# Performance work log

Hardware: AMD Instinct MI355X
Metric: run time of the kernel (lower is better)

Reference implementation:

```python
import jax, jax.numpy as jnp
import numpy as np
from jax import lax

B, T, V, D, H = 32, 128, 32000, 512, 512


def setup_inputs() -> dict:
    key = jax.random.key(0)
    ks = jax.random.split(key, 8)
    s = 0.05  # keep gate pre-activations in a sane range
    return {
        "dst": jax.random.randint(ks[0], (B, T), 0, V),
        "E": jax.random.normal(ks[1], (V, D), jnp.float32) * s,
        "W_ih": jax.random.normal(ks[2], (4 * H, D + H), jnp.float32) * s,
        "W_hh": jax.random.normal(ks[3], (4 * H, H), jnp.float32) * s,
        "b_ih": jnp.zeros((4 * H,), jnp.float32),
        "b_hh": jnp.zeros((4 * H,), jnp.float32),
        "h0": jax.random.normal(ks[4], (B, H), jnp.float32) * s,
        "c0": jax.random.normal(ks[5], (B, H), jnp.float32) * s,
        "out0": jax.random.normal(ks[6], (B, H), jnp.float32) * s,
    }


def reference(dst, E, W_ih, W_hh, b_ih, b_hh, h0, c0, out0):
    # Embed targets: [B, T, D] -> time-major [T, B, D]
    emb_tbd = jnp.swapaxes(E[dst], 0, 1)

    def step(carry, e_t):
        h, c, out_prev = carry
        # input feeding: concat embedding with previous output -> [B, D+H]
        x = jnp.concatenate([e_t, out_prev], axis=1)
        gates = x @ W_ih.T + b_ih + h @ W_hh.T + b_hh  # [B, 4H]
        i, f, g, o = jnp.split(gates, 4, axis=1)
        i = jax.nn.sigmoid(i)
        f = jax.nn.sigmoid(f)
        g = jnp.tanh(g)
        o = jax.nn.sigmoid(o)
        c_new = f * c + i * g
        h_new = o * jnp.tanh(c_new)
        # attn is identity; dropout disabled (p=0 / eval)
        return (h_new, c_new, h_new), h_new

    _, outs_tbh = lax.scan(step, (h0, c0, out0), emb_tbd)  # [T, B, H]
    out_bth = jnp.swapaxes(outs_tbh, 0, 1)  # [B, T, H]
    # weight-tied projection to vocab + log softmax
    logits = jnp.einsum("bth,vh->btv", out_bth, E)  # [B, T, V]
    return jax.nn.log_softmax(logits, axis=-1)
```

## Files before the change

### kernel.cpp

```cpp
#include <hip/hip_runtime.h>
#include <hip/hip_bf16.h>
#include <math.h>

#define B_ 32
#define T_ 128
#define V_ 32000
#define D_ 512
#define H_ 512

typedef __attribute__((ext_vector_type(8))) short bf16x8;
typedef __attribute__((ext_vector_type(8))) unsigned short u16x8;
typedef __attribute__((ext_vector_type(4))) float f32x4;
typedef __attribute__((ext_vector_type(2))) unsigned long long u64x2;

#define AS1 __attribute__((address_space(1)))
#define AS3 __attribute__((address_space(3)))

__device__ __forceinline__ unsigned short f2bf(float x) {
  unsigned int b = __float_as_uint(x);
  return (unsigned short)((b + 0x7FFFu + ((b >> 16) & 1u)) >> 16);
}
__device__ __forceinline__ float bf2f(unsigned short u) {
  return __uint_as_float(((unsigned int)u) << 16);
}
__device__ __forceinline__ float sigm(float x) { return 1.0f / (1.0f + __expf(-x)); }
__device__ __forceinline__ float tanh_fast(float x) { return 1.0f - 2.0f / (__expf(2.0f * x) + 1.0f); }

__device__ __forceinline__ unsigned long long ald64(const unsigned long long* p) {
  return __hip_atomic_load(p, __ATOMIC_RELAXED, __HIP_MEMORY_SCOPE_AGENT);
}
__device__ __forceinline__ unsigned ald32(const unsigned* p) {
  return __hip_atomic_load(p, __ATOMIC_RELAXED, __HIP_MEMORY_SCOPE_AGENT);
}

__global__ __launch_bounds__(64) void embed_bf_kernel(const int* __restrict__ dst,
                                                      const float* __restrict__ E,
                                                      unsigned short* __restrict__ embbf) {
  int rt = blockIdx.x;
  int t = rt >> 5, b = rt & 31;
  int v = dst[b * T_ + t];
  const float4* src = (const float4*)(E + (size_t)v * D_);
  ushort4* d = (ushort4*)(embbf + (size_t)rt * D_);
  #pragma unroll
  for (int r = 0; r < 2; ++r) {
    float4 x = src[threadIdx.x + r * 64];
    ushort4 o; o.x = f2bf(x.x); o.y = f2bf(x.y); o.z = f2bf(x.z); o.w = f2bf(x.w);
    d[threadIdx.x + r * 64] = o;
  }
}

__global__ void cvt_kernel(const float* __restrict__ in, unsigned short* __restrict__ out, int n4) {
  int stride = gridDim.x * blockDim.x;
  for (int i = blockIdx.x * blockDim.x + threadIdx.x; i < n4; i += stride) {
    float4 v = ((const float4*)in)[i];
    ushort4 o; o.x = f2bf(v.x); o.y = f2bf(v.y); o.z = f2bf(v.z); o.w = f2bf(v.w);
    ((ushort4*)out)[i] = o;
  }
}

__global__ void cvt_w1_kernel(const float* __restrict__ Wih, unsigned short* __restrict__ W1bf, int n4) {
  int stride = gridDim.x * blockDim.x;
  for (int i = blockIdx.x * blockDim.x + threadIdx.x; i < n4; i += stride) {
    int flat = i * 4;
    int r = flat >> 9, c = flat & 511;
    float4 v = *(const float4*)(Wih + (size_t)r * 1024 + c);
    ushort4 o; o.x = f2bf(v.x); o.y = f2bf(v.y); o.z = f2bf(v.z); o.w = f2bf(v.w);
    ((ushort4*)W1bf)[i] = o;
  }
}

__global__ void wr_prep_swz_kernel(const float* __restrict__ Wih, const float* __restrict__ Whh,
                                   unsigned short* __restrict__ Wrs, int n4) {
  int stride = gridDim.x * blockDim.x;
  for (int i = blockIdx.x * blockDim.x + threadIdx.x; i < n4; i += stride) {
    int flat = i * 4;
    int grow = flat >> 9, k = flat & 511;
    float4 a = *(const float4*)(Wih + (size_t)grow * 1024 + 512 + k);
    float4 b = ((const float4*)Whh)[i];
    ushort4 o;
    o.x = f2bf(a.x + b.x); o.y = f2bf(a.y + b.y); o.z = f2bf(a.z + b.z); o.w = f2bf(a.w + b.w);
    int gate = grow >> 9, kgl = grow & 511;
    int orow = (kgl >> 5) * 128 + (kgl & 31) * 4 + gate;
    int chunk = (k >> 3) ^ (orow & 7);
    *(ushort4*)(Wrs + (size_t)orow * 512 + chunk * 8 + (k & 7)) = o;
  }
}

__global__ __launch_bounds__(256) void gemm_pre_kernel(
    const unsigned short* __restrict__ A,
    const unsigned short* __restrict__ Bm,
    const float* __restrict__ bih, const float* __restrict__ bhh,
    unsigned short* __restrict__ preA3)
{
  __shared__ unsigned short ldsA[2][128 * 32];
  __shared__ unsigned short ldsB[2][128 * 32];
  const int tid = threadIdx.x;
  const int lane = tid & 63;
  const int wid = tid >> 6;
  const int wm = wid >> 1, wn = wid & 1;
  const int m0 = blockIdx.y * 128;
  const int n0 = blockIdx.x * 128;
  const int srow = lane >> 2;
  const int scol = (lane & 3) * 8;

  f32x4 acc[4][4] = {};
  const int NK = 512 / 32;

  auto stage = [&](int kk, int buf) {
    const int k0 = kk * 32;
    #pragma unroll
    for (int c = 0; c < 2; ++c) {
      const int r = wid * 32 + c * 16;
      const unsigned short* sa = A  + (size_t)(m0 + r + srow) * 512 + k0 + scol;
      const unsigned short* sb = Bm + (size_t)(n0 + r + srow) * 512 + k0 + scol;
      __builtin_amdgcn_global_load_lds((const AS1 void*)sa, (AS3 void*)&ldsA[buf][r * 32], 16, 0, 0);
      __builtin_amdgcn_global_load_lds((const AS1 void*)sb, (AS3 void*)&ldsB[buf][r * 32], 16, 0, 0);
    }
  };

  stage(0, 0);
  __syncthreads();

  const int rl = lane & 15;
  const int kb = lane >> 4;

  for (int kk = 0; kk < NK; ++kk) {
    const int buf = kk & 1;
    if (kk + 1 < NK) stage(kk + 1, buf ^ 1);
    const bf16x8* Af = (const bf16x8*)&ldsA[buf][0];
    const bf16x8* Bf = (const bf16x8*)&ldsB[buf][0];
    bf16x8 av[4], bv[4];
    #pragma unroll
    for (int mi = 0; mi < 4; ++mi) av[mi] = Af[(wm * 64 + mi * 16 + rl) * 4 + kb];
    #pragma unroll
    for (int ni = 0; ni < 4; ++ni) bv[ni] = Bf[(wn * 64 + ni * 16 + rl) * 4 + kb];
    #pragma unroll
    for (int mi = 0; mi < 4; ++mi)
      #pragma unroll
      for (int ni = 0; ni < 4; ++ni)
        acc[mi][ni] = __builtin_amdgcn_mfma_f32_16x16x32_bf16(av[mi], bv[ni], acc[mi][ni], 0, 0, 0);
    __syncthreads();
  }

  const int rb = (lane >> 4) * 4;
  #pragma unroll
  for (int mi = 0; mi < 4; ++mi)
    #pragma unroll
    for (int ni = 0; ni < 4; ++ni) {
      int mbase = m0 + wm * 64 + mi * 16 + rb;
      int col   = n0 + wn * 64 + ni * 16 + rl;
      int gate = col >> 9, kg = col & 511;
      int tt = mbase >> 5, bb0 = mbase & 31;
      float bb = bih[col] + bhh[col];
      #pragma unroll
      for (int j = 0; j < 4; ++j)
        preA3[(((size_t)tt * 512 + kg) * 32 + bb0 + j) * 4 + gate] = f2bf(acc[mi][ni][j] + bb);
    }
}

__global__ __launch_bounds__(256) void delta0_kernel(const float* __restrict__ Wih,
                                                     const float* __restrict__ out0,
                                                     const float* __restrict__ h0,
                                                     unsigned short* __restrict__ preA3) {
  const int r = blockIdx.x;
  const int tid = threadIdx.x;
  const int b = tid >> 3, seg = tid & 7;
  __shared__ float red[32][9];
  const float4* o4 = (const float4*)(out0 + (size_t)b * 512 + seg * 64);
  const float4* h4 = (const float4*)(h0 + (size_t)b * 512 + seg * 64);
  const float4* w4 = (const float4*)(Wih + (size_t)r * 1024 + 512 + seg * 64);
  float s = 0.f;
  #pragma unroll
  for (int j = 0; j < 16; ++j) {
    float4 o = o4[j], h = h4[j], w = w4[j];
    s += (o.x - h.x) * w.x + (o.y - h.y) * w.y + (o.z - h.z) * w.z + (o.w - h.w) * w.w;
  }
  red[b][seg] = s;
  __syncthreads();
  if (tid < 32) {
    float t = 0.f;
    #pragma unroll
    for (int j = 0; j < 8; ++j) t += red[tid][j];
    int gate = r >> 9, kgl = r & 511;
    unsigned short* p = preA3 + ((size_t)kgl * 32 + tid) * 4 + gate;
    *p = f2bf(bf2f(*p) + t);
  }
}

__global__ __launch_bounds__(1024) void lstm_persist_rs_kernel(
    const unsigned short* __restrict__ Wrs,
    const unsigned short* __restrict__ preA3,
    const float* __restrict__ c0,
    unsigned short* __restrict__ hb0,
    unsigned short* __restrict__ hb1,
    unsigned short* __restrict__ Abf,
    unsigned int* __restrict__ flags)
{
  __shared__ unsigned short wlds[128 * 512];
  __shared__ __align__(16) char hexch[2][16 * 1024];
  const int tid = threadIdx.x, bid = blockIdx.x;
  const int lane = tid & 63, wid = tid >> 6;

  #pragma unroll
  for (int it = 0; it < 8; ++it) {
    int r = it * 16 + wid;
    const unsigned short* src = Wrs + ((size_t)bid * 128 + r) * 512 + lane * 8;
    __builtin_amdgcn_global_load_lds((const AS1 void*)src, (AS3 void*)&wlds[r * 512], 16, 0, 0);
  }

  const int myhalf = wid >> 3;
  const int rt = wid & 7;
  const int q = lane >> 4, rl = lane & 15;
  const int kg = bid * 32 + rt * 4 + q;
  const int b = myhalf * 16 + rl;
  float c_reg = c0[(size_t)b * 512 + kg];

  const int row = rt * 16 + rl;
  const char* wbase = (const char*)wlds + row * 1024;
  const int rx = (row & 7) << 4;
  const int hx = (rl & 7) << 4;

  const int sw = wid & 7;
  const int sr = sw * 2 + (lane >> 5);
  const int sc = lane & 31;
  const int sblk = sc >> 1;
  const int srx = (sr & 7) << 4;
  const int sofs = sc * 32;

  if (myhalf == 0) {
    const unsigned long long* src =
        (const unsigned long long*)(hb0 + (size_t)sr * 512) + sc * 4;
    unsigned long long d0 = ald64(src + 0), d1 = ald64(src + 1);
    unsigned long long d2 = ald64(src + 2), d3 = ald64(src + 3);
    char* dst = hexch[0] + sr * 1024;
    u64x2 w0; w0[0] = d0; w0[1] = d1;
    u64x2 w1; w1[0] = d2; w1[1] = d3;
    *(u64x2*)(dst + (sofs ^ srx)) = w0;
    *(u64x2*)(dst + ((sofs + 16) ^ srx)) = w1;
  }
  __syncthreads();

  for (int p = 0; p < 2 * T_; ++p) {
    const int t = p >> 1, ph = p & 1, buf = p & 1;

    if (myhalf == ph) {
      unsigned long long pre =
          *(const unsigned long long*)(preA3 + (((size_t)t * 512 + kg) * 32 + b) * 4);
      const char* hbase = hexch[buf] + rl * 1024;
      f32x4 acc = {}, acc2 = {};
      #pragma unroll
      for (int kk = 0; kk < 16; kk += 2) {
        int k0 = kk * 32 + q * 8;
        int k1 = k0 + 32;
        bf16x8 av0 = *(const bf16x8*)(wbase + ((k0 * 2) ^ rx));
        bf16x8 bv0 = *(const bf16x8*)(hbase + ((k0 * 2) ^ hx));
        bf16x8 av1 = *(const bf16x8*)(wbase + ((k1 * 2) ^ rx));
        bf16x8 bv1 = *(const bf16x8*)(hbase + ((k1 * 2) ^ hx));
        acc  = __builtin_amdgcn_mfma_f32_16x16x32_bf16(av0, bv0, acc, 0, 0, 0);
        acc2 = __builtin_amdgcn_mfma_f32_16x16x32_bf16(av1, bv1, acc2, 0, 0, 0);
      }
      float g0 = acc[0] + acc2[0] + bf2f((unsigned short)(pre));
      float g1 = acc[1] + acc2[1] + bf2f((unsigned short)(pre >> 16));
      float g2 = acc[2] + acc2[2] + bf2f((unsigned short)(pre >> 32));
      float g3 = acc[3] + acc2[3] + bf2f((unsigned short)(pre >> 48));
      float iv = sigm(g0), fv = sigm(g1), gv = tanh_fast(g2), ov = sigm(g3);
      float cn = fv * c_reg + iv * gv;
      c_reg = cn;
      float hn = ov * tanh_fast(cn);
      int hv = (int)f2bf(hn);
      int nb = __shfl(hv, lane + 16);
      if ((q & 1) == 0) {
        unsigned pair = (unsigned)hv | ((unsigned)nb << 16);
        if (t != T_ - 1) {
          unsigned short* hout = ((t + 1) & 1) ? hb1 : hb0;
          __hip_atomic_store((unsigned int*)(hout + (size_t)b * 512 + kg), pair,
                             __ATOMIC_RELAXED, __HIP_MEMORY_SCOPE_AGENT);
        }
        *(unsigned*)(Abf + ((size_t)b * T_ + t) * 512 + kg) = pair;
      }
    } else if (p + 1 < 2 * T_) {
      const int t2 = (p + 1) >> 1;
      if (t2 > 0) {
        const unsigned* fl = &flags[(myhalf * 16 + sblk) * 16];
        unsigned spins = 0;
        while (ald32(fl) < (unsigned)t2) {
          if (++spins > 1000000u) break;
        }
      }
      const unsigned short* hsrc = (t2 & 1) ? hb1 : hb0;
      const unsigned long long* src =
          (const unsigned long long*)(hsrc + (size_t)(myhalf * 16 + sr) * 512) + sc * 4;
      unsigned long long d0 = ald64(src + 0), d1 = ald64(src + 1);
      unsigned long long d2 = ald64(src + 2), d3 = ald64(src + 3);
      char* dst = hexch[buf ^ 1] + sr * 1024;
      u64x2 w0; w0[0] = d0; w0[1] = d1;
      u64x2 w1; w1[0] = d2; w1[1] = d3;
      *(u64x2*)(dst + (sofs ^ srx)) = w0;
      *(u64x2*)(dst + ((sofs + 16) ^ srx)) = w1;
    }

    __syncthreads();

    if (tid == ph * 512)
      __hip_atomic_store(&flags[(ph * 16 + bid) * 16], (unsigned)(t + 1),
                         __ATOMIC_RELAXED, __HIP_MEMORY_SCOPE_AGENT);
  }
}

__global__ __launch_bounds__(256) void gemm_kernel(
    const unsigned short* __restrict__ A,
    const unsigned short* __restrict__ Bm,
    float* __restrict__ C,
    unsigned short* __restrict__ Cbf,
    int use_bf,
    float* __restrict__ pmax, float* __restrict__ psum)
{
  __shared__ unsigned short ldsA[2][128 * 32];
  __shared__ unsigned short ldsB[2][128 * 32];
  __shared__ float smax[2][128];
  __shared__ float ssum[2][128];
  const int tid = threadIdx.x;
  const int lane = tid & 63;
  const int wid = tid >> 6;
  const int wm = wid >> 1, wn = wid & 1;
  const int m0 = blockIdx.x * 128;
  const int n0 = blockIdx.y * 128;
  const int srow = lane >> 2;

  f32x4 acc[4][4] = {};
  const int NK = 512 / 32;

  auto stage = [&](int kk, int buf) {
    const int k0 = kk * 32;
    const int sw = (srow >> 1) & 3;
    const int gc = ((lane & 3) ^ sw) * 8;
    #pragma unroll
    for (int c = 0; c < 2; ++c) {
      const int r = wid * 32 + c * 16;
      const unsigned short* sa = A  + (size_t)(m0 + r + srow) * 512 + k0 + gc;
      const unsigned short* sb = Bm + (size_t)(n0 + r + srow) * 512 + k0 + gc;
      __builtin_amdgcn_global_load_lds((const AS1 void*)sa, (AS3 void*)&ldsA[buf][r * 32], 16, 0, 0);
      __builtin_amdgcn_global_load_lds((const AS1 void*)sb, (AS3 void*)&ldsB[buf][r * 32], 16, 0, 0);
    }
  };

  stage(0, 0);
  __syncthreads();

  const int rl = lane & 15;
  const int kb = lane >> 4;
  const int rsw = kb ^ ((rl >> 1) & 3);

  for (int kk = 0; kk < NK; ++kk) {
    const int buf = kk & 1;
    if (kk + 1 < NK) stage(kk + 1, buf ^ 1);
    const bf16x8* Af = (const bf16x8*)&ldsA[buf][0];
    const bf16x8* Bf = (const bf16x8*)&ldsB[buf][0];
    bf16x8 av[4], bv[4];
    #pragma unroll
    for (int mi = 0; mi < 4; ++mi) av[mi] = Af[(wm * 64 + mi * 16 + rl) * 4 + rsw];
    #pragma unroll
    for (int ni = 0; ni < 4; ++ni) bv[ni] = Bf[(wn * 64 + ni * 16 + rl) * 4 + rsw];
    #pragma unroll
    for (int mi = 0; mi < 4; ++mi)
      #pragma unroll
      for (int ni = 0; ni < 4; ++ni)
        acc[mi][ni] = __builtin_amdgcn_mfma_f32_16x16x32_bf16(av[mi], bv[ni], acc[mi][ni], 0, 0, 0);
    __syncthreads();
  }

  const int rb = kb * 4;
  if (use_bf) {
    #pragma unroll
    for (int mi = 0; mi < 4; ++mi)
      #pragma unroll
      for (int ni = 0; ni < 4; ++ni) {
        size_t rrow = (size_t)(m0 + wm * 64 + mi * 16 + rb);
        size_t col = (size_t)(n0 + wn * 64 + ni * 16 + rl);
        #pragma unroll
        for (int j = 0; j < 4; ++j)
          __builtin_nontemporal_store(f2bf(acc[mi][ni][j]), &Cbf[(rrow + j) * (size_t)V_ + col]);
      }
  } else {
    #pragma unroll
    for (int mi = 0; mi < 4; ++mi)
      #pragma unroll
      for (int ni = 0; ni < 4; ++ni) {
        size_t rrow = (size_t)(m0 + wm * 64 + mi * 16 + rb);
        size_t col = (size_t)(n0 + wn * 64 + ni * 16 + rl);
        #pragma unroll
        for (int j = 0; j < 4; ++j)
          __builtin_nontemporal_store(acc[mi][ni][j], &C[(rrow + j) * (size_t)V_ + col]);
      }
  }

  float tm[4][4];
  #pragma unroll
  for (int mi = 0; mi < 4; ++mi)
    #pragma unroll
    for (int j = 0; j < 4; ++j) {
      float m = fmaxf(fmaxf(acc[mi][0][j], acc[mi][1][j]), fmaxf(acc[mi][2][j], acc[mi][3][j]));
      m = fmaxf(m, __shfl_xor(m, 1)); m = fmaxf(m, __shfl_xor(m, 2));
      m = fmaxf(m, __shfl_xor(m, 4)); m = fmaxf(m, __shfl_xor(m, 8));
      tm[mi][j] = m;
    }
  if (rl == 0) {
    #pragma unroll
    for (int mi = 0; mi < 4; ++mi)
      #pragma unroll
      for (int j = 0; j < 4; ++j)
        smax[wn][wm * 64 + mi * 16 + kb * 4 + j] = tm[mi][j];
  }
  __syncthreads();
  float ts[4][4];
  #pragma unroll
  for (int mi = 0; mi < 4; ++mi)
    #pragma unroll
    for (int j = 0; j < 4; ++j) {
      int rlocal = wm * 64 + mi * 16 + kb * 4 + j;
      float M = fmaxf(smax[0][rlocal], smax[1][rlocal]);
      float s = __expf(acc[mi][0][j] - M) + __expf(acc[mi][1][j] - M) +
                __expf(acc[mi][2][j] - M) + __expf(acc[mi][3][j] - M);
      s += __shfl_xor(s, 1); s += __shfl_xor(s, 2);
      s += __shfl_xor(s, 4); s += __shfl_xor(s, 8);
      ts[mi][j] = s;
    }
  if (rl == 0) {
    #pragma unroll
    for (int mi = 0; mi < 4; ++mi)
      #pragma unroll
      for (int j = 0; j < 4; ++j)
        ssum[wn][wm * 64 + mi * 16 + kb * 4 + j] = ts[mi][j];
  }
  __syncthreads();
  if (tid < 128) {
    float M = fmaxf(smax[0][tid], smax[1][tid]);
    float S = ssum[0][tid] + ssum[1][tid];
    pmax[(size_t)(m0 + tid) * 256 + blockIdx.y] = M;
    psum[(size_t)(m0 + tid) * 256 + blockIdx.y] = S;
  }
}

__device__ __forceinline__ float lse_from_partials(const float* pmax, const float* psum,
                                                   size_t row, int tid, int lane, int wid,
                                                   float* red) {
  float pm = (tid < 250) ? pmax[row * 256 + tid] : -INFINITY;
  float ps = (tid < 250) ? psum[row * 256 + tid] : 0.f;

  float m = pm;
  #pragma unroll
  for (int off = 32; off > 0; off >>= 1) m = fmaxf(m, __shfl_xor(m, off));
  if (lane == 0) red[wid] = m;
  __syncthreads();
  m = fmaxf(fmaxf(red[0], red[1]), fmaxf(red[2], red[3]));
  __syncthreads();

  float s = (tid < 250) ? ps * __expf(pm - m) : 0.f;
  #pragma unroll
  for (int off = 32; off > 0; off >>= 1) s += __shfl_xor(s, off);
  if (lane == 0) red[wid] = s;
  __syncthreads();
  s = red[0] + red[1] + red[2] + red[3];
  return m + logf(s);
}

__global__ __launch_bounds__(256) void softmax_finish_bf_kernel(
    const unsigned short* __restrict__ Cbf, float* __restrict__ C,
    const float* __restrict__ pmax, const float* __restrict__ psum) {
  const size_t row = blockIdx.x;
  const int tid = threadIdx.x, lane = tid & 63, wid = tid >> 6;
  __shared__ float red[4];
  const float lse = lse_from_partials(pmax, psum, row, tid, lane, wid, red);

  const u16x8* pb = (const u16x8*)(Cbf + row * (size_t)V_);
  f32x4* pf = (f32x4*)(C + row * (size_t)V_);
  for (int i = tid; i < 4000; i += 256) {
    u16x8 v = __builtin_nontemporal_load(&pb[i]);
    f32x4 lo, hi;
    lo[0] = bf2f(v[0]) - lse; lo[1] = bf2f(v[1]) - lse;
    lo[2] = bf2f(v[2]) - lse; lo[3] = bf2f(v[3]) - lse;
    hi[0] = bf2f(v[4]) - lse; hi[1] = bf2f(v[5]) - lse;
    hi[2] = bf2f(v[6]) - lse; hi[3] = bf2f(v[7]) - lse;
    __builtin_nontemporal_store(lo, &pf[i * 2]);
    __builtin_nontemporal_store(hi, &pf[i * 2 + 1]);
  }
}

__global__ __launch_bounds__(256) void softmax_finish_kernel(
    float* __restrict__ C, const float* __restrict__ pmax, const float* __restrict__ psum) {
  const size_t row = blockIdx.x;
  const int tid = threadIdx.x, lane = tid & 63, wid = tid >> 6;
  __shared__ float red[4];
  const float lse = lse_from_partials(pmax, psum, row, tid, lane, wid, red);

  f32x4* p4 = (f32x4*)(C + row * (size_t)V_);
  for (int i = tid; i < 8000; i += 256) {
    f32x4 v = p4[i];
    v -= lse;
    __builtin_nontemporal_store(v, &p4[i]);
  }
}

extern "C" void kernel_launch(void* const* d_in, const int* in_sizes, int n_in,
                              void* d_out, int out_size, void* d_ws, size_t ws_size,
                              hipStream_t stream) {
  const int*   dst  = (const int*)d_in[0];
  const float* E    = (const float*)d_in[1];
  const float* Wih  = (const float*)d_in[2];
  const float* Whh  = (const float*)d_in[3];
  const float* bih  = (const float*)d_in[4];
  const float* bhh  = (const float*)d_in[5];
  const float* h0   = (const float*)d_in[6];
  const float* c0   = (const float*)d_in[7];
  const float* out0 = (const float*)d_in[8];
  float* C = (float*)d_out;

  char* ws = (char*)d_ws;
  unsigned short* Ebf   = (unsigned short*)(ws);
  unsigned short* preA3 = (unsigned short*)(ws + (size_t)33554432);
  unsigned short* Wrs   = (unsigned short*)(ws + (size_t)50331648);
  unsigned short* embbf = (unsigned short*)(ws + (size_t)52428800);
  float*          pmax  = (float*)(ws + (size_t)52428800);
  unsigned short* W1bf  = (unsigned short*)(ws + (size_t)56623104);
  float*          psum  = (float*)(ws + (size_t)56623104);
  unsigned short* Abf   = (unsigned short*)(ws + (size_t)60817408);
  unsigned short* hb0   = (unsigned short*)(ws + (size_t)65011712);
  unsigned short* hb1   = (unsigned short*)(ws + (size_t)65044480);
  unsigned int*   flg   = (unsigned int*)(ws + (size_t)65077248);
  unsigned short* Cbf   = (unsigned short*)(ws + (size_t)65079296);

  const int use_bf = (ws_size >= (size_t)65079296 + (size_t)B_ * T_ * V_ * 2) ? 1 : 0;

  (void)hipMemsetAsync(flg, 0, 2048, stream);

  embed_bf_kernel<<<dim3(T_ * B_), dim3(64), 0, stream>>>(dst, E, embbf);
  cvt_kernel<<<dim3(2048), dim3(256), 0, stream>>>(E, Ebf, V_ * D_ / 4);
  cvt_w1_kernel<<<dim3(256), dim3(256), 0, stream>>>(Wih, W1bf, 2048 * 512 / 4);
  wr_prep_swz_kernel<<<dim3(256), dim3(256), 0, stream>>>(Wih, Whh, Wrs, 2048 * 512 / 4);

  gemm_pre_kernel<<<dim3(2048 / 128, 4096 / 128), dim3(256), 0, stream>>>(embbf, W1bf, bih, bhh, preA3);
  delta0_kernel<<<dim3(2048), dim3(256), 0, stream>>>(Wih, out0, h0, preA3);
  cvt_kernel<<<dim3(16), dim3(256), 0, stream>>>(h0, hb0, B_ * H_ / 4);

  lstm_persist_rs_kernel<<<dim3(16), dim3(1024), 0, stream>>>(Wrs, preA3, c0, hb0, hb1, Abf, flg);

  gemm_kernel<<<dim3(32, 250), dim3(256), 0, stream>>>(Abf, Ebf, C, Cbf, use_bf, pmax, psum);
  if (use_bf)
    softmax_finish_bf_kernel<<<dim3(B_ * T_), dim3(256), 0, stream>>>(Cbf, C, pmax, psum);
  else
    softmax_finish_kernel<<<dim3(B_ * T_), dim3(256), 0, stream>>>(C, pmax, psum);
}
```

Measured before the change: 1.108 ms.

## Chunk logits GEMM and softmax finish so bf16 intermediate stays cache-resident

Splits the vocab projection GEMM and the log-softmax finish pass into row chunks sized to the available workspace. Each chunk writes its bf16 logits into a smaller scratch buffer, which is then read back immediately. Stores and loads are now regular rather than nontemporal, so the intermediate can hit in the last-level cache instead of going to HBM. The cost is extra kernel launches and smaller per-launch grids. It also lets the bf16 path run when the workspace is too small for the full intermediate.

```diff
diff --git a/kernel.cpp b/kernel.cpp
--- a/kernel.cpp
+++ b/kernel.cpp
@@ -312,7 +312,7 @@
     const unsigned short* __restrict__ Bm,
     float* __restrict__ C,
     unsigned short* __restrict__ Cbf,
-    int use_bf,
+    int row0, int use_bf,
     float* __restrict__ pmax, float* __restrict__ psum)
 {
   __shared__ unsigned short ldsA[2][128 * 32];
@@ -323,7 +323,8 @@
   const int lane = tid & 63;
   const int wid = tid >> 6;
   const int wm = wid >> 1, wn = wid & 1;
-  const int m0 = blockIdx.x * 128;
+  const int lm0 = blockIdx.x * 128;
+  const int m0 = row0 + lm0;
   const int n0 = blockIdx.y * 128;
   const int srow = lane >> 2;
 
@@ -375,11 +376,11 @@
     for (int mi = 0; mi < 4; ++mi)
       #pragma unroll
       for (int ni = 0; ni < 4; ++ni) {
-        size_t rrow = (size_t)(m0 + wm * 64 + mi * 16 + rb);
+        size_t lrow = (size_t)(lm0 + wm * 64 + mi * 16 + rb);
         size_t col = (size_t)(n0 + wn * 64 + ni * 16 + rl);
         #pragma unroll
         for (int j = 0; j < 4; ++j)
-          __builtin_nontemporal_store(f2bf(acc[mi][ni][j]), &Cbf[(rrow + j) * (size_t)V_ + col]);
+          Cbf[(lrow + j) * (size_t)V_ + col] = f2bf(acc[mi][ni][j]);
       }
   } else {
     #pragma unroll
@@ -465,17 +466,17 @@
 }
 
 __global__ __launch_bounds__(256) void softmax_finish_bf_kernel(
-    const unsigned short* __restrict__ Cbf, float* __restrict__ C,
+    const unsigned short* __restrict__ Cbf, float* __restrict__ C, int row0,
     const float* __restrict__ pmax, const float* __restrict__ psum) {
-  const size_t row = blockIdx.x;
+  const size_t row = (size_t)row0 + blockIdx.x;
   const int tid = threadIdx.x, lane = tid & 63, wid = tid >> 6;
   __shared__ float red[4];
   const float lse = lse_from_partials(pmax, psum, row, tid, lane, wid, red);
 
-  const u16x8* pb = (const u16x8*)(Cbf + row * (size_t)V_);
+  const u16x8* pb = (const u16x8*)(Cbf + (size_t)blockIdx.x * V_);
   f32x4* pf = (f32x4*)(C + row * (size_t)V_);
   for (int i = tid; i < 4000; i += 256) {
-    u16x8 v = __builtin_nontemporal_load(&pb[i]);
+    u16x8 v = pb[i];
     f32x4 lo, hi;
     lo[0] = bf2f(v[0]) - lse; lo[1] = bf2f(v[1]) - lse;
     lo[2] = bf2f(v[2]) - lse; lo[3] = bf2f(v[3]) - lse;
@@ -527,9 +528,14 @@
   unsigned short* hb0   = (unsigned short*)(ws + (size_t)65011712);
   unsigned short* hb1   = (unsigned short*)(ws + (size_t)65044480);
   unsigned int*   flg   = (unsigned int*)(ws + (size_t)65077248);
-  unsigned short* Cbf   = (unsigned short*)(ws + (size_t)65079296);
-
-  const int use_bf = (ws_size >= (size_t)65079296 + (size_t)B_ * T_ * V_ * 2) ? 1 : 0;
+  const size_t cbf_off  = 65079296;
+  unsigned short* Cbf   = (unsigned short*)(ws + cbf_off);
+
+  const size_t avail = (ws_size > cbf_off) ? ws_size - cbf_off : 0;
+  int chunk = 0;
+  if      (avail >= (size_t)2048 * V_ * 2) chunk = 2048;
+  else if (avail >= (size_t)1024 * V_ * 2) chunk = 1024;
+  else if (avail >= (size_t)512  * V_ * 2) chunk = 512;
 
   (void)hipMemsetAsync(flg, 0, 2048, stream);
 
@@ -544,9 +550,16 @@
 
   lstm_persist_rs_kernel<<<dim3(16), dim3(1024), 0, stream>>>(Wrs, preA3, c0, hb0, hb1, Abf, flg);
 
-  gemm_kernel<<<dim3(32, 250), dim3(256), 0, stream>>>(Abf, Ebf, C, Cbf, use_bf, pmax, psum);
-  if (use_bf)
-    softmax_finish_bf_kernel<<<dim3(B_ * T_), dim3(256), 0, stream>>>(Cbf, C, pmax, psum);
-  else
+  if (chunk) {
+    for (int r0 = 0; r0 < B_ * T_; r0 += chunk) {
+      gemm_kernel<<<dim3(chunk / 128, V_ / 128), dim3(256), 0, stream>>>(
+          Abf, Ebf, C, Cbf, r0, 1, pmax, psum);
+      softmax_finish_bf_kernel<<<dim3(chunk), dim3(256), 0, stream>>>(
+          Cbf, C, r0, pmax, psum);
+    }
+  } else {
+    gemm_kernel<<<dim3((B_ * T_) / 128, V_ / 128), dim3(256), 0, stream>>>(
+        Abf, Ebf, C, Cbf, 0, 0, pmax, psum);
     softmax_finish_kernel<<<dim3(B_ * T_), dim3(256), 0, stream>>>(C, pmax, psum);
-}
+  }
+}
```

Measured after the change: 1.104 ms. Within noise of the previous version (-0.4%).
